# Optimization experiments

Measured on AMD Instinct MI355X. Metric: run time of the kernel, lower is better.

## Reference

```python
import jax, jax.numpy as jnp
import numpy as np

N = 40000
E = 640000
IN = 128
H = 8
F = 16  # out_features per head; H*F == IN for the residual
NEG_SLOPE = 0.2
BN_EPS = 1e-5
SOFTMAX_EPS = 1e-16


def setup_inputs() -> dict:
    key = jax.random.key(0)
    ks = jax.random.split(key, 7)
    x = jax.random.normal(ks[0], (N, IN), dtype=jnp.float32)
    edge_index = jax.random.randint(ks[1], (2, E), 0, N, dtype=jnp.int32)
    # GATConv parameters (glorot-ish scale)
    W = jax.random.normal(ks[2], (IN, H * F), dtype=jnp.float32) * (1.0 / np.sqrt(IN))
    att_src = jax.random.normal(ks[3], (H, F), dtype=jnp.float32) * (1.0 / np.sqrt(F))
    att_dst = jax.random.normal(ks[4], (H, F), dtype=jnp.float32) * (1.0 / np.sqrt(F))
    bias = jnp.zeros((H * F,), dtype=jnp.float32)
    bn_gamma = jnp.ones((H * F,), dtype=jnp.float32)
    bn_beta = jnp.zeros((H * F,), dtype=jnp.float32)
    return {"x": x, "edge_index": edge_index, "W": W, "att_src": att_src,
            "att_dst": att_dst, "bias": bias, "bn_gamma": bn_gamma, "bn_beta": bn_beta}


def _gat_layer(x, src, dst, W, att_src, att_dst, bias, bn_gamma, bn_beta):
    n = x.shape[0]
    xp = (x @ W).reshape(n, H, F)                      # [N,H,F] transformed features
    a_s = jnp.einsum('nhf,hf->nh', xp, att_src)        # [N,H]
    a_d = jnp.einsum('nhf,hf->nh', xp, att_dst)
    e = jax.nn.leaky_relu(a_s[src] + a_d[dst], NEG_SLOPE)   # [E,H] per-edge logits
    # segment softmax over edges sharing the same destination node
    m = jax.ops.segment_max(e, dst, num_segments=n)    # [N,H]
    m = jnp.where(jnp.isfinite(m), m, 0.0)             # guard isolated nodes
    p = jnp.exp(e - m[dst])
    s = jax.ops.segment_sum(p, dst, num_segments=n)    # [N,H]
    alpha = p / (s[dst] + SOFTMAX_EPS)                 # [E,H]
    # scatter-aggregate messages
    msg = alpha[:, :, None] * xp[src]                  # [E,H,F]
    out = jax.ops.segment_sum(msg, dst, num_segments=n)  # [N,H,F]
    h = out.reshape(n, H * F) + bias
    # BatchNorm1d (training-mode batch statistics, biased variance)
    mean = h.mean(axis=0)
    var = h.var(axis=0)
    h = (h - mean) * jax.lax.rsqrt(var + BN_EPS) * bn_gamma + bn_beta
    h = jax.nn.relu(h)
    return h + x                                        # residual (dropout p=0 -> identity)


def reference(x, edge_index, W, att_src, att_dst, bias, bn_gamma, bn_beta):
    n = x.shape[0]
    loops = jnp.arange(n, dtype=edge_index.dtype)
    src = jnp.concatenate([edge_index[0], loops])       # add self-loops (GATConv default)
    dst = jnp.concatenate([edge_index[1], loops])
    return _gat_layer(x, src, dst, W, att_src, att_dst, bias, bn_gamma, bn_beta)
```

## Files before the change

kernel.cpp:

```cpp
#include <hip/hip_runtime.h>
#include <math.h>


constexpr float NEG_SLOPE = 0.2f;
constexpr float BN_EPS = 1e-5f;
constexpr float SM_EPS = 1e-16f;
constexpr int SLOTS = 96;

typedef __attribute__((ext_vector_type(8))) short short8;
typedef __attribute__((ext_vector_type(4))) float f32x4;

__device__ inline unsigned bf16rne(float f) {
    unsigned b = __float_as_uint(f);
    return (b + 0x7fffu + ((b >> 16) & 1u)) >> 16;
}

__global__ __launch_bounds__(256) void k_init(
    const float* __restrict__ W, const float* __restrict__ att_src,
    const float* __restrict__ att_dst, unsigned short* __restrict__ Wtg,
    int* __restrict__ zbase, int zcount)
{
    int b = blockIdx.x;
    if (b < 64) {
        int idx = b * 256 + threadIdx.x;
        int k = idx >> 7, nc = idx & 127;
        Wtg[nc * 128 + k] = (unsigned short)bf16rne(W[idx]);
    } else if (b < 72) {
        int c = (b - 64) * 16 + (threadIdx.x >> 4);
        int j = threadIdx.x & 15;
        int h = j & 7;
        const float* att = (j < 8) ? att_src : att_dst;
        float v = 0.f;
#pragma unroll
        for (int f = 0; f < 16; ++f)
            v += W[c * 128 + h * 16 + f] * att[h * 16 + f];
        Wtg[(128 + j) * 128 + c] = (unsigned short)bf16rne(v);
    } else {
        int idx = (b - 72) * 256 + threadIdx.x;
        if (idx < zcount) zbase[idx] = 0;
    }
}

__global__ __launch_bounds__(256) void k_gemm(
    const float* __restrict__ x, const unsigned short* __restrict__ Wtg,
    const int* __restrict__ ei, int E,
    unsigned* __restrict__ xpb, float* __restrict__ a_s, float* __restrict__ a_d,
    int* __restrict__ deg, unsigned short* __restrict__ csr_src, int n)
{
    {
        const int xcd = blockIdx.x & 7;
        const int crank = blockIdx.x >> 3;
        const int cblocks = gridDim.x >> 3;
        const int nodes_per = (n + 7) >> 3;
        const int dlo = xcd * nodes_per;
        const int dhi = min(n, dlo + nodes_per);
        const int tot = E + n;
        const int stride = cblocks * 256;
        for (int e = crank * 256 + threadIdx.x; e < tot; e += stride) {
            int dst = (e < E) ? ei[E + e] : (e - E);
            if (dst < dlo || dst >= dhi) continue;
            int src = (e < E) ? ei[e] : dst;
            int slot = atomicAdd(&deg[dst], 1);
            csr_src[(size_t)dst * SLOTS + slot] = (unsigned short)src;
        }
    }

    const int ntiles = (n + 63) >> 6;
    if ((int)blockIdx.x >= ntiles) return;

    const int tid = threadIdx.x;
    const int lane = tid & 63;
    const int wid = tid >> 6;
    const int quad = lane >> 4;
    const int l16 = lane & 15;
    const int row = blockIdx.x * 64 + wid * 16 + l16;

    const float4* x4 = (const float4*)x;
    short8 afrag[4];
#pragma unroll
    for (int kt = 0; kt < 4; ++kt) {
        float4 f0 = make_float4(0.f, 0.f, 0.f, 0.f), f1 = f0;
        if (row < n) {
            f0 = x4[(size_t)row * 32 + kt * 8 + quad * 2];
            f1 = x4[(size_t)row * 32 + kt * 8 + quad * 2 + 1];
        }
        short8 a;
        a[0] = (short)bf16rne(f0.x); a[1] = (short)bf16rne(f0.y);
        a[2] = (short)bf16rne(f0.z); a[3] = (short)bf16rne(f0.w);
        a[4] = (short)bf16rne(f1.x); a[5] = (short)bf16rne(f1.y);
        a[6] = (short)bf16rne(f1.z); a[7] = (short)bf16rne(f1.w);
        afrag[kt] = a;
    }

    f32x4 acc[9];
#pragma unroll
    for (int ct = 0; ct < 9; ++ct) acc[ct] = (f32x4){0.f, 0.f, 0.f, 0.f};

#pragma unroll
    for (int ct = 0; ct < 9; ++ct) {
#pragma unroll
        for (int kt = 0; kt < 4; ++kt) {
            short8 b = *(const short8*)&Wtg[(size_t)(ct * 16 + l16) * 128 + kt * 32 + quad * 8];
            acc[ct] = __builtin_amdgcn_mfma_f32_16x16x32_bf16(afrag[kt], b, acc[ct], 0, 0, 0);
        }
    }

    const int rowbase = blockIdx.x * 64 + wid * 16 + quad * 4;
#pragma unroll
    for (int ct = 0; ct < 8; ++ct) {
#pragma unroll
        for (int r = 0; r < 4; ++r) {
            float val = acc[ct][r];
            float other = __shfl_xor(val, 1);
            int orow = rowbase + r;
            if (!(lane & 1) && orow < n) {
                unsigned u = bf16rne(val) | (bf16rne(other) << 16);
                xpb[(size_t)orow * 64 + ct * 8 + (l16 >> 1)] = u;
            }
        }
    }
#pragma unroll
    for (int r = 0; r < 4; ++r) {
        int orow = rowbase + r;
        if (orow < n) {
            float val = acc[8][r];
            if (l16 < 8) a_s[(size_t)orow * 8 + l16] = val;
            else         a_d[(size_t)orow * 8 + (l16 - 8)] = val;
        }
    }
}

__global__ __launch_bounds__(256) void k_gather(
    const int* __restrict__ deg, const unsigned short* __restrict__ csr_src,
    const float* __restrict__ a_s, const float* __restrict__ a_d,
    const unsigned* __restrict__ xpb, unsigned* __restrict__ aggb, int n)
{
    int node = blockIdx.x * 4 + (threadIdx.x >> 6);
    if (node >= n) return;
    int lane = threadIdx.x & 63;
    int h = lane >> 3;
    float ad = a_d[(size_t)node * 8 + h];
    const unsigned short* rowp = csr_src + (size_t)node * SLOTS;
    int cnt = deg[node];
    float acc0 = 0.f, acc1 = 0.f, s = 0.f;

    for (int slot = 0; slot < cnt; slot += 8) {
        int sx[8]; float w[8]; unsigned u[8];
#pragma unroll
        for (int j = 0; j < 8; ++j) {
            int sj = slot + j;
            sx[j] = rowp[sj < cnt ? sj : cnt - 1];
        }
#pragma unroll
        for (int j = 0; j < 8; ++j) w[j] = a_s[(size_t)sx[j] * 8 + h];
#pragma unroll
        for (int j = 0; j < 8; ++j) u[j] = xpb[(size_t)sx[j] * 64 + lane];
#pragma unroll
        for (int j = 0; j < 8; ++j) {
            float v = w[j] + ad;
            v = v > 0.f ? v : NEG_SLOPE * v;
            float p = __expf(v);
            p = (slot + j < cnt) ? p : 0.f;
            s += p;
            acc0 = fmaf(p, __uint_as_float(u[j] << 16), acc0);
            acc1 = fmaf(p, __uint_as_float(u[j] & 0xffff0000u), acc1);
        }
    }
    float inv = 1.0f / (s + SM_EPS);
    aggb[(size_t)node * 64 + lane] = bf16rne(acc0 * inv) | (bf16rne(acc1 * inv) << 16);
}

__global__ __launch_bounds__(256) void k_bnstats(
    const unsigned* __restrict__ aggb, int n, float* __restrict__ stats)
{
    __shared__ float red[4][256];
    const int cp = threadIdx.x & 63;
    const int rg = threadIdx.x >> 6;
    float s0 = 0.f, s1 = 0.f, q0 = 0.f, q1 = 0.f;
    for (int r = blockIdx.x * 4 + rg; r < n; r += gridDim.x * 4) {
        unsigned u = aggb[(size_t)r * 64 + cp];
        float v0 = __uint_as_float(u << 16);
        float v1 = __uint_as_float(u & 0xffff0000u);
        s0 += v0; q0 += v0 * v0;
        s1 += v1; q1 += v1 * v1;
    }
    red[rg][cp * 2] = s0;       red[rg][cp * 2 + 1] = s1;
    red[rg][128 + cp * 2] = q0; red[rg][128 + cp * 2 + 1] = q1;
    __syncthreads();
    int idx = threadIdx.x;
    float v = red[0][idx] + red[1][idx] + red[2][idx] + red[3][idx];
    if (idx < 128) atomicAdd(&stats[idx], v);
    else           atomicAdd(&stats[128 + (idx - 128)], v);
}

__global__ __launch_bounds__(256) void k_final(
    const unsigned* __restrict__ aggb, const float* __restrict__ gamma,
    const float* __restrict__ beta, const float* __restrict__ stats,
    const float* __restrict__ x, float* __restrict__ out, int n)
{
    int i4 = blockIdx.x * 256 + threadIdx.x;
    int total4 = n * 32;
    if (i4 >= total4) return;
    int c4 = (i4 & 31) * 4;
    float invn = 1.0f / (float)n;
    uint2 au = ((const uint2*)aggb)[i4];
    float av[4] = { __uint_as_float(au.x << 16), __uint_as_float(au.x & 0xffff0000u),
                    __uint_as_float(au.y << 16), __uint_as_float(au.y & 0xffff0000u) };
    float4 xv = ((const float4*)x)[i4];
    float4 o;
#pragma unroll
    for (int j = 0; j < 4; ++j) {
        int c = c4 + j;
        float mean = stats[c] * invn;
        float var = stats[128 + c] * invn - mean * mean;
        float v = (av[j] - mean) * rsqrtf(var + BN_EPS) * gamma[c] + beta[c];
        v = fmaxf(v, 0.f);
        (&o.x)[j] = v + (&xv.x)[j];
    }
    ((float4*)out)[i4] = o;
}

extern "C" void kernel_launch(void* const* d_in, const int* in_sizes, int n_in,
                              void* d_out, int out_size, void* d_ws, size_t ws_size,
                              hipStream_t stream)
{
    const float* x        = (const float*)d_in[0];
    const int*   ei       = (const int*)d_in[1];
    const float* W        = (const float*)d_in[2];
    const float* att_src  = (const float*)d_in[3];
    const float* att_dst  = (const float*)d_in[4];
    const float* bn_gamma = (const float*)d_in[6];
    const float* bn_beta  = (const float*)d_in[7];
    float* out = (float*)d_out;

    const int n = in_sizes[0] / 128;
    const int E = in_sizes[1] / 2;

    float*          stats   = (float*)d_ws;
    int*            deg     = (int*)(stats + 256);
    unsigned short* csr_src = (unsigned short*)(deg + n);
    unsigned short* Wtg     = csr_src + (size_t)n * SLOTS;
    unsigned*       xpb     = (unsigned*)(Wtg + 144 * 128);
    unsigned*       aggb    = xpb + (size_t)n * 64;
    float*          a_s     = (float*)(aggb + (size_t)n * 64);
    float*          a_d     = a_s + (size_t)n * 8;

    const int zcount = 256 + n;
    const int ginit = 72 + (zcount + 255) / 256;
    int ggemm = 3200;
    ggemm = (ggemm + 7) & ~7;

    k_init<<<ginit, 256, 0, stream>>>(W, att_src, att_dst, Wtg, (int*)stats, zcount);
    k_gemm<<<ggemm, 256, 0, stream>>>(x, Wtg, ei, E, xpb, a_s, a_d,
                                      deg, csr_src, n);
    k_gather<<<(n + 3) / 4, 256, 0, stream>>>(deg, csr_src, a_s, a_d, xpb, aggb, n);
    k_bnstats<<<640, 256, 0, stream>>>(aggb, n, stats);
    k_final<<<(n * 32 + 255) / 256, 256, 0, stream>>>(aggb, bn_gamma, bn_beta,
                                                      stats, x, out, n);
}
```

Before: 180.3 us.

## Split CSR build and GEMM into separate block roles with vectorized edge loads

Blocks in the fused GEMM kernel now take one of two roles. The first ntiles blocks do only the feature GEMM, and a fixed set of extra blocks build the destination-bucketed CSR. Before, every block first ran the edge-scatter loop and then the GEMM tiles ran after it. The edge loop now reads src and dst indices four at a time with int4 loads, and self-loops go in a separate node loop. This is meant to let the GEMM run alongside the scatter instead of after it, and to cut index load instructions. In exchange, the edge work now sits on fewer blocks, and the int4 loads assume E is a multiple of 4 and the index buffers are 16-byte aligned.

New measurement: 177.1 us. About the same (-1.8%).

```diff
diff --git a/kernel.cpp b/kernel.cpp
--- a/kernel.cpp
+++ b/kernel.cpp
@@ -6,6 +6,7 @@
 constexpr float BN_EPS = 1e-5f;
 constexpr float SM_EPS = 1e-16f;
 constexpr int SLOTS = 96;
+constexpr int EBLOCKS = 1416;
 
 typedef __attribute__((ext_vector_type(8))) short short8;
 typedef __attribute__((ext_vector_type(4))) float f32x4;
@@ -45,28 +46,41 @@
     const float* __restrict__ x, const unsigned short* __restrict__ Wtg,
     const int* __restrict__ ei, int E,
     unsigned* __restrict__ xpb, float* __restrict__ a_s, float* __restrict__ a_d,
-    int* __restrict__ deg, unsigned short* __restrict__ csr_src, int n)
-{
-    {
+    int* __restrict__ deg, unsigned short* __restrict__ csr_src, int n,
+    int ntiles)
+{
+    if ((int)blockIdx.x >= ntiles) {
         const int xcd = blockIdx.x & 7;
-        const int crank = blockIdx.x >> 3;
-        const int cblocks = gridDim.x >> 3;
+        const int crank = (blockIdx.x - ntiles) >> 3;
+        const int cpb = EBLOCKS >> 3;
         const int nodes_per = (n + 7) >> 3;
         const int dlo = xcd * nodes_per;
         const int dhi = min(n, dlo + nodes_per);
-        const int tot = E + n;
-        const int stride = cblocks * 256;
-        for (int e = crank * 256 + threadIdx.x; e < tot; e += stride) {
-            int dst = (e < E) ? ei[E + e] : (e - E);
-            if (dst < dlo || dst >= dhi) continue;
-            int src = (e < E) ? ei[e] : dst;
-            int slot = atomicAdd(&deg[dst], 1);
-            csr_src[(size_t)dst * SLOTS + slot] = (unsigned short)src;
-        }
-    }
-
-    const int ntiles = (n + 63) >> 6;
-    if ((int)blockIdx.x >= ntiles) return;
+        const int t = crank * 256 + threadIdx.x;
+        const int estride = cpb * 256 * 4;
+        for (int e = t * 4; e < E; e += estride) {
+            int4 d4 = *(const int4*)(ei + E + e);
+            int4 s4 = *(const int4*)(ei + e);
+            int ds[4] = {d4.x, d4.y, d4.z, d4.w};
+            int ss[4] = {s4.x, s4.y, s4.z, s4.w};
+#pragma unroll
+            for (int j = 0; j < 4; ++j) {
+                int dst = ds[j];
+                if (dst >= dlo && dst < dhi) {
+                    int slot = atomicAdd(&deg[dst], 1);
+                    csr_src[(size_t)dst * SLOTS + slot] = (unsigned short)ss[j];
+                }
+            }
+        }
+        const int nstride = cpb * 256;
+        for (int node = t; node < n; node += nstride) {
+            if (node >= dlo && node < dhi) {
+                int slot = atomicAdd(&deg[node], 1);
+                csr_src[(size_t)node * SLOTS + slot] = (unsigned short)node;
+            }
+        }
+        return;
+    }
 
     const int tid = threadIdx.x;
     const int lane = tid & 63;
@@ -247,12 +261,12 @@
 
     const int zcount = 256 + n;
     const int ginit = 72 + (zcount + 255) / 256;
-    int ggemm = 3200;
-    ggemm = (ggemm + 7) & ~7;
+    const int ntiles = (n + 63) >> 6;
+    const int ggemm = ntiles + EBLOCKS;
 
     k_init<<<ginit, 256, 0, stream>>>(W, att_src, att_dst, Wtg, (int*)stats, zcount);
     k_gemm<<<ggemm, 256, 0, stream>>>(x, Wtg, ei, E, xpb, a_s, a_d,
-                                      deg, csr_src, n);
+                                      deg, csr_src, n, ntiles);
     k_gather<<<(n + 3) / 4, 256, 0, stream>>>(deg, csr_src, a_s, a_d, xpb, aggb, n);
     k_bnstats<<<640, 256, 0, stream>>>(aggb, n, stats);
     k_final<<<(n * 32 + 255) / 256, 256, 0, stream>>>(aggb, bn_gamma, bn_beta,
```
